# Optimization experiments

Hardware: AMD Instinct MI355X
Metric: run time of the kernel (lower is better)

The kernel has to match this reference:

```python
import jax, jax.numpy as jnp
import numpy as np

VOCAB, EMB, HID, NCLS = 50257, 48, 128, 2000
B, S = 512, 1024


def setup_inputs() -> dict:
    key = jax.random.key(0)
    ks = jax.random.split(key, 8)
    x = jax.random.randint(ks[0], (B, S), 0, VOCAB)
    emb_table = jax.random.normal(ks[1], (VOCAB, EMB), dtype=jnp.float32)
    emb_table = emb_table.at[0].set(0.0)  # padding_idx=0
    k_ih = 1.0 / np.sqrt(HID)
    w_ih = jax.random.uniform(ks[2], (4 * HID, EMB), minval=-k_ih, maxval=k_ih, dtype=jnp.float32)
    w_hh = jax.random.uniform(ks[3], (4 * HID, HID), minval=-k_ih, maxval=k_ih, dtype=jnp.float32)
    b_ih = jax.random.uniform(ks[4], (4 * HID,), minval=-k_ih, maxval=k_ih, dtype=jnp.float32)
    b_hh = jax.random.uniform(ks[5], (4 * HID,), minval=-k_ih, maxval=k_ih, dtype=jnp.float32)
    k_fc = 1.0 / np.sqrt(HID)
    w_fc = jax.random.uniform(ks[6], (NCLS, HID), minval=-k_fc, maxval=k_fc, dtype=jnp.float32)
    b_fc = jax.random.uniform(ks[7], (NCLS,), minval=-k_fc, maxval=k_fc, dtype=jnp.float32)
    return {"x": x, "emb_table": emb_table, "w_ih": w_ih, "w_hh": w_hh,
            "b_ih": b_ih, "b_hh": b_hh, "w_fc": w_fc, "b_fc": b_fc}


def _lstm_last_hidden(e, w_ih, w_hh, b_ih, b_hh):
    # e: [B, S, E]. Precompute input contributions for all timesteps (one big GEMM).
    xg = jnp.einsum('bse,ge->bsg', e, w_ih) + b_ih + b_hh  # [B, S, 4H]
    xg = jnp.transpose(xg, (1, 0, 2))                      # [S, B, 4H]
    Bn = e.shape[0]
    h0 = jnp.zeros((Bn, HID), e.dtype)
    c0 = jnp.zeros((Bn, HID), e.dtype)

    def step(carry, xg_t):
        h, c = carry
        g = xg_t + h @ w_hh.T                              # [B, 4H]
        i, f, gg, o = jnp.split(g, 4, axis=-1)             # PyTorch gate order i,f,g,o
        i = jax.nn.sigmoid(i)
        f = jax.nn.sigmoid(f)
        gg = jnp.tanh(gg)
        o = jax.nn.sigmoid(o)
        c = f * c + i * gg
        h = o * jnp.tanh(c)
        return (h, c), None

    (h_n, _), _ = jax.lax.scan(step, (h0, c0), xg)
    return h_n


def reference(x, emb_table, w_ih, w_hh, b_ih, b_hh, w_fc, b_fc):
    e = emb_table[x]                                       # [B, S, E] gather
    h_n = _lstm_last_hidden(e, w_ih, w_hh, b_ih, b_hh)     # [B, H]
    return h_n @ w_fc.T + b_fc                             # [B, NCLS]
```

## Files before the change

kernel.cpp:

```cpp
#include <hip/hip_runtime.h>

#define DI __device__ __forceinline__

typedef unsigned int uint;
typedef unsigned short ushort;
typedef _Float16 half2t __attribute__((ext_vector_type(2)));

#define VOCAB 50257
#define NEMB 48
#define HID 128
#define G4 512
#define NCLS 2000
#define BATCH 512
#define SEQ 1024

#if __has_builtin(__builtin_amdgcn_fdot2)
DI float fdot2(half2t a, half2t b, float c) { return __builtin_amdgcn_fdot2(a, b, c, false); }
#else
DI float fdot2(half2t a, half2t b, float c) { return c + (float)a.x * (float)b.x + (float)a.y * (float)b.y; }
#endif

#define LOG2E 1.4426950408889634f

DI float dppx1(float v) {
  return __builtin_bit_cast(float,
      __builtin_amdgcn_update_dpp(0, __builtin_bit_cast(int, v), 0xB1, 0xF, 0xF, true));
}
DI float dppx2(float v) {
  return __builtin_bit_cast(float,
      __builtin_amdgcn_update_dpp(0, __builtin_bit_cast(int, v), 0x4E, 0xF, 0xF, true));
}
DI float dppb3(float v) {
  return __builtin_bit_cast(float,
      __builtin_amdgcn_update_dpp(0, __builtin_bit_cast(int, v), 0xFF, 0xF, 0xF, true));
}

#define VROWS 32
__global__ __launch_bounds__(512) void build_P(
    const float* __restrict__ emb, const float* __restrict__ w_ih,
    const float* __restrict__ b_ih, const float* __restrict__ b_hh,
    ushort* __restrict__ P3)
{
  __shared__ __align__(16) float eL[VROWS][NEMB];
  const int tid = threadIdx.x;
  const int v0 = blockIdx.x * VROWS;
  int nrows = VOCAB - v0; if (nrows > VROWS) nrows = VROWS;

  for (int f = tid; f < nrows * NEMB; f += 512)
    eL[f / NEMB][f % NEMB] = emb[(size_t)v0 * NEMB + f];

  float w[NEMB];
  {
    const float* wr = w_ih + (size_t)tid * NEMB;
#pragma unroll
    for (int k = 0; k < NEMB; k++) w[k] = wr[k];
  }
  float bias = b_ih[tid] + b_hh[tid];
  __syncthreads();

  for (int v = 0; v < nrows; v++) {
    const float4* e4 = (const float4*)&eL[v][0];
    float a = bias;
#pragma unroll
    for (int k = 0; k < NEMB / 4; k++) {
      float4 e = e4[k];
      a += w[4 * k] * e.x + w[4 * k + 1] * e.y + w[4 * k + 2] * e.z + w[4 * k + 3] * e.w;
    }
    P3[(size_t)(v0 + v) * G4 + tid] = __builtin_bit_cast(ushort, (_Float16)a);
  }
}

template<bool USE_P>
__global__ __launch_bounds__(512, 4) void lstm_scan(
    const int* __restrict__ x, const float* __restrict__ emb,
    const float* __restrict__ w_ih, const float* __restrict__ w_hh,
    const float* __restrict__ b_ih, const float* __restrict__ b_hh,
    const ushort* __restrict__ P3, float* __restrict__ hout)
{
  __shared__ int tokL[SEQ];
  __shared__ __align__(16) _Float16 h16[2][HID];
  __shared__ __align__(8) half2t e16[2][NEMB / 2];

  const int tid = threadIdx.x;
  const int b   = blockIdx.x;
  const int u   = tid >> 2;
  const int q   = tid & 3;
  const bool par1 = (q & 1) != 0;
  const bool par2 = (q & 2) != 0;
  const int goff = (q << 7) + u;

  const bool isg = (q == 2);
  const float mk = isg ? (2.0f * LOG2E) : (-LOG2E);
  const float av = isg ? -2.0f : 1.0f;
  const float bv = isg ? 1.0f : 0.0f;

  {
    const int* xp = x + (size_t)b * SEQ;
    tokL[tid] = xp[tid];
    tokL[tid + 512] = xp[tid + 512];
  }

  half2t w[4][16];
#pragma unroll
  for (int g = 0; g < 4; g++) {
    const float4* wr = (const float4*)(w_hh + (size_t)(g * HID + u) * HID + 32 * q);
#pragma unroll
    for (int k4 = 0; k4 < 8; k4++) {
      float4 v = wr[k4];
      half2t p;
      p.x = (_Float16)v.x; p.y = (_Float16)v.y; w[g][2 * k4] = p;
      p.x = (_Float16)v.z; p.y = (_Float16)v.w; w[g][2 * k4 + 1] = p;
    }
  }

  half2t wihq[NEMB / 2];
  float biasq = 0.0f;
  if (!USE_P) {
    const float* wr = w_ih + (size_t)(q * HID + u) * NEMB;
#pragma unroll
    for (int k = 0; k < NEMB / 2; k++) {
      half2t p; p.x = (_Float16)wr[2 * k]; p.y = (_Float16)wr[2 * k + 1];
      wihq[k] = p;
    }
    biasq = b_ih[q * HID + u] + b_hh[q * HID + u];
  }
  if (tid < HID) h16[1][tid] = (_Float16)0.0f;
  __syncthreads();

  float c = 0.0f;
  ushort pa = 0, pb = 0;
  float2 einfl = {0.0f, 0.0f};
  if (USE_P) {
    pa = P3[(size_t)tokL[0] * G4 + goff];
    pb = P3[(size_t)tokL[1] * G4 + goff];
  } else {
    if (tid < NEMB / 2) {
      float2 e0 = ((const float2*)(emb + (size_t)tokL[0] * NEMB))[tid];
      einfl     = ((const float2*)(emb + (size_t)tokL[1] * NEMB))[tid];
      half2t p; p.x = (_Float16)e0.x; p.y = (_Float16)e0.y;
      e16[0][tid] = p;
    }
    __syncthreads();
  }

#define STEP(t, par) do {                                                      \
    int tc = (t) + 2; if (tc > SEQ - 1) tc = SEQ - 1;                          \
    int tn = tokL[tc];                                                         \
    ushort cur = (par) ? pb : pa;                                              \
    if (USE_P) {                                                               \
      ushort nx = P3[(size_t)tn * G4 + goff];                \
      if ((par) == 0) pa = nx; else pb = nx;                                   \
    } else {                                                                   \
      if (tid < NEMB / 2) {                                                    \
        half2t p; p.x = (_Float16)einfl.x; p.y = (_Float16)einfl.y;            \
        e16[((t) + 1) & 1][tid] = p;                                           \
        einfl = ((const float2*)(emb + (size_t)tn * NEMB))[tid];               \
      }                                                                        \
    }                                                                          \
    const uint4* hv = (const uint4*)(&h16[(par) ^ 1][32 * q]);                 \
    float a0 = 0.f, a1 = 0.f, a2 = 0.f, a3 = 0.f;                              \
    _Pragma("unroll")                                                          \
    for (int q4 = 0; q4 < 4; q4++) {                                           \
      uint4 hq = hv[q4];                                                       \
      half2t h0 = __builtin_bit_cast(half2t, hq.x);                            \
      half2t h1 = __builtin_bit_cast(half2t, hq.y);                            \
      half2t h2 = __builtin_bit_cast(half2t, hq.z);                            \
      half2t h3 = __builtin_bit_cast(half2t, hq.w);                            \
      a0 = fdot2(w[0][4*q4+0], h0, a0); a1 = fdot2(w[1][4*q4+0], h0, a1);      \
      a2 = fdot2(w[2][4*q4+0], h0, a2); a3 = fdot2(w[3][4*q4+0], h0, a3);      \
      a0 = fdot2(w[0][4*q4+1], h1, a0); a1 = fdot2(w[1][4*q4+1], h1, a1);      \
      a2 = fdot2(w[2][4*q4+1], h1, a2); a3 = fdot2(w[3][4*q4+1], h1, a3);      \
      a0 = fdot2(w[0][4*q4+2], h2, a0); a1 = fdot2(w[1][4*q4+2], h2, a1);      \
      a2 = fdot2(w[2][4*q4+2], h2, a2); a3 = fdot2(w[3][4*q4+2], h2, a3);      \
      a0 = fdot2(w[0][4*q4+3], h3, a0); a1 = fdot2(w[1][4*q4+3], h3, a1);      \
      a2 = fdot2(w[2][4*q4+3], h3, a2); a3 = fdot2(w[3][4*q4+3], h3, a3);      \
    }                                                                          \
                       \
    float kA = par1 ? a1 : a0, sA = par1 ? a0 : a1; kA += dppx1(sA);           \
    float kB = par1 ? a3 : a2, sB = par1 ? a2 : a3; kB += dppx1(sB);           \
    float kF = par2 ? kB : kA, sF = par2 ? kA : kB; kF += dppx2(sF);           \
    float xg;                                                                  \
    if (USE_P) {                                                               \
      xg = (float)__builtin_bit_cast(_Float16, cur);                           \
    } else {                                                                   \
      xg = biasq;                                                              \
      _Pragma("unroll")                                                        \
      for (int k = 0; k < NEMB / 2; k++) xg = fdot2(wihq[k], e16[(par)][k], xg);\
    }                                                                          \
    float gv = kF + xg;                                                        \
    float act = av * __builtin_amdgcn_rcpf(                                    \
                    __builtin_amdgcn_exp2f(mk * gv) + 1.0f) + bv;              \
    float gt = dppx2(act);                                 \
    float sf = dppx1(act);                                \
    c = act * gt + sf * c;                                \
    float tanhc = 1.0f - 2.0f * __builtin_amdgcn_rcpf(                         \
                    __builtin_amdgcn_exp2f(2.0f * LOG2E * c) + 1.0f);          \
    float so = dppb3(act);                            \
    float hh = so * tanhc;                                \
    if (q == 0) {                                                              \
      h16[(par)][u] = (_Float16)hh;                                            \
      if ((t) == SEQ - 1) hout[(size_t)b * HID + u] = hh;                      \
    }                                                                          \
    __syncthreads();                                                           \
  } while (0)

  for (int t = 0; t < SEQ; t += 2) { STEP(t, 0); STEP(t + 1, 1); }
#undef STEP
}

#define FCR 64
#define FCC 64
__global__ __launch_bounds__(256) void fc_kernel(
    const float* __restrict__ h, const float* __restrict__ w_fc,
    const float* __restrict__ b_fc, float* __restrict__ out)
{
  __shared__ float aT[HID][FCR];
  __shared__ float bT[HID][FCC];
  const int tid = threadIdx.x;
  const int r0 = blockIdx.y * FCR;
  const int c0 = blockIdx.x * FCC;

  for (int f = tid; f < FCR * (HID / 4); f += 256) {
    int row = f >> 5, qq = f & 31;
    float4 v = ((const float4*)h)[(((size_t)(r0 + row)) << 5) + qq];
    aT[4 * qq + 0][row] = v.x; aT[4 * qq + 1][row] = v.y;
    aT[4 * qq + 2][row] = v.z; aT[4 * qq + 3][row] = v.w;
    int wrow = c0 + row;
    float4 wv;
    if (wrow < NCLS) wv = ((const float4*)w_fc)[(((size_t)wrow) << 5) + qq];
    else { wv.x = 0.f; wv.y = 0.f; wv.z = 0.f; wv.w = 0.f; }
    bT[4 * qq + 0][row] = wv.x; bT[4 * qq + 1][row] = wv.y;
    bT[4 * qq + 2][row] = wv.z; bT[4 * qq + 3][row] = wv.w;
  }
  __syncthreads();

  const int cr = tid & 15, rr = tid >> 4;
  float acc[4][4];
#pragma unroll
  for (int i = 0; i < 4; i++)
#pragma unroll
    for (int j = 0; j < 4; j++) acc[i][j] = 0.0f;

#pragma unroll 4
  for (int k = 0; k < HID; k++) {
    float4 av = *(const float4*)&aT[k][4 * rr];
    float4 bv = *(const float4*)&bT[k][4 * cr];
    float a[4] = {av.x, av.y, av.z, av.w};
    float bb[4] = {bv.x, bv.y, bv.z, bv.w};
#pragma unroll
    for (int i = 0; i < 4; i++)
#pragma unroll
      for (int j = 0; j < 4; j++) acc[i][j] += a[i] * bb[j];
  }

#pragma unroll
  for (int j = 0; j < 4; j++) {
    int cc = c0 + 4 * cr + j;
    if (cc < NCLS) {
      float bias = b_fc[cc];
#pragma unroll
      for (int i = 0; i < 4; i++)
        out[(size_t)(r0 + 4 * rr + i) * NCLS + cc] = acc[i][j] + bias;
    }
  }
}

extern "C" void kernel_launch(void* const* d_in, const int* in_sizes, int n_in,
                              void* d_out, int out_size, void* d_ws, size_t ws_size,
                              hipStream_t stream) {
  const int*   xx   = (const int*)d_in[0];
  const float* emb  = (const float*)d_in[1];
  const float* w_ih = (const float*)d_in[2];
  const float* w_hh = (const float*)d_in[3];
  const float* b_ih = (const float*)d_in[4];
  const float* b_hh = (const float*)d_in[5];
  const float* w_fc = (const float*)d_in[6];
  const float* b_fc = (const float*)d_in[7];
  float* out = (float*)d_out;

  const size_t pbytes = (size_t)VOCAB * G4 * sizeof(ushort);
  const size_t palign = (pbytes + 255) & ~(size_t)255;
  const size_t hbytes = (size_t)BATCH * HID * sizeof(float);

  float* hout;
  if (ws_size >= palign + hbytes) {
    ushort* P3 = (ushort*)d_ws;
    hout = (float*)((char*)d_ws + palign);
    build_P<<<(VOCAB + VROWS - 1) / VROWS, 512, 0, stream>>>(emb, w_ih, b_ih, b_hh, P3);
    lstm_scan<true><<<BATCH, 512, 0, stream>>>(xx, emb, w_ih, w_hh, b_ih, b_hh, P3, hout);
  } else {
    hout = (float*)d_ws;
    lstm_scan<false><<<BATCH, 512, 0, stream>>>(xx, emb, w_ih, w_hh, b_ih, b_hh,
                                                (const ushort*)nullptr, hout);
  }
  dim3 fcg((NCLS + FCC - 1) / FCC, BATCH / FCR);
  fc_kernel<<<fcg, 256, 0, stream>>>(hout, w_fc, b_fc, out);
}
```

Baseline: 1.017 ms.

## Deepen P3 gather prefetch to four steps and use LDS-only barrier

The LSTM scan now prefetches the precomputed input-gate values four timesteps ahead instead of two, rotating through four registers in a loop unrolled by four. The token array is padded so the prefetch index needs no clamp. The per-step __syncthreads is replaced by an inline-asm barrier that waits only on LDS counters (lgkmcnt), so the outstanding global gather is not drained at every step. This hides more gather latency on the serial recurrence, but relies on the asm barrier being correct for the shared-memory h exchange and uses more registers.

```diff
diff --git a/kernel.cpp b/kernel.cpp
--- a/kernel.cpp
+++ b/kernel.cpp
@@ -34,6 +34,8 @@
   return __builtin_bit_cast(float,
       __builtin_amdgcn_update_dpp(0, __builtin_bit_cast(int, v), 0xFF, 0xF, 0xF, true));
 }
+
+DI void bar_lds() { asm volatile("s_waitcnt lgkmcnt(0)\n\ts_barrier" ::: "memory"); }
 
 #define VROWS 32
 __global__ __launch_bounds__(512) void build_P(
@@ -77,7 +79,7 @@
     const float* __restrict__ b_ih, const float* __restrict__ b_hh,
     const ushort* __restrict__ P3, float* __restrict__ hout)
 {
-  __shared__ int tokL[SEQ];
+  __shared__ int tokPad[SEQ + 4];
   __shared__ __align__(16) _Float16 h16[2][HID];
   __shared__ __align__(8) half2t e16[2][NEMB / 2];
 
@@ -96,8 +98,9 @@
 
   {
     const int* xp = x + (size_t)b * SEQ;
-    tokL[tid] = xp[tid];
-    tokL[tid + 512] = xp[tid + 512];
+    tokPad[tid] = xp[tid];
+    tokPad[tid + 512] = xp[tid + 512];
+    if (tid < 4) tokPad[SEQ + tid] = xp[SEQ - 1];
   }
 
   half2t w[4][16];
@@ -128,36 +131,36 @@
   __syncthreads();
 
   float c = 0.0f;
-  ushort pa = 0, pb = 0;
+  ushort pr0 = 0, pr1 = 0, pr2 = 0, pr3 = 0;
   float2 einfl = {0.0f, 0.0f};
   if (USE_P) {
-    pa = P3[(size_t)tokL[0] * G4 + goff];
-    pb = P3[(size_t)tokL[1] * G4 + goff];
+    pr0 = P3[(size_t)tokPad[0] * G4 + goff];
+    pr1 = P3[(size_t)tokPad[1] * G4 + goff];
+    pr2 = P3[(size_t)tokPad[2] * G4 + goff];
+    pr3 = P3[(size_t)tokPad[3] * G4 + goff];
   } else {
     if (tid < NEMB / 2) {
-      float2 e0 = ((const float2*)(emb + (size_t)tokL[0] * NEMB))[tid];
-      einfl     = ((const float2*)(emb + (size_t)tokL[1] * NEMB))[tid];
+      float2 e0 = ((const float2*)(emb + (size_t)tokPad[0] * NEMB))[tid];
+      einfl     = ((const float2*)(emb + (size_t)tokPad[1] * NEMB))[tid];
       half2t p; p.x = (_Float16)e0.x; p.y = (_Float16)e0.y;
       e16[0][tid] = p;
     }
     __syncthreads();
   }
 
-#define STEP(t, par) do {                                                      \
-    int tc = (t) + 2; if (tc > SEQ - 1) tc = SEQ - 1;                          \
-    int tn = tokL[tc];                                                         \
-    ushort cur = (par) ? pb : pa;                                              \
+#define STEP(tt, jpar, PRJ) do {                                               \
+    ushort cur = PRJ;                                                          \
     if (USE_P) {                                                               \
-      ushort nx = P3[(size_t)tn * G4 + goff];                \
-      if ((par) == 0) pa = nx; else pb = nx;                                   \
+      int tn4 = tokPad[(tt) + 4];                                              \
+      PRJ = P3[(size_t)tn4 * G4 + goff];           \
     } else {                                                                   \
       if (tid < NEMB / 2) {                                                    \
         half2t p; p.x = (_Float16)einfl.x; p.y = (_Float16)einfl.y;            \
-        e16[((t) + 1) & 1][tid] = p;                                           \
-        einfl = ((const float2*)(emb + (size_t)tn * NEMB))[tid];               \
+        e16[((tt) + 1) & 1][tid] = p;                                          \
+        einfl = ((const float2*)(emb + (size_t)tokPad[(tt) + 2] * NEMB))[tid]; \
       }                                                                        \
     }                                                                          \
-    const uint4* hv = (const uint4*)(&h16[(par) ^ 1][32 * q]);                 \
+    const uint4* hv = (const uint4*)(&h16[((jpar) + 1) & 1][32 * q]);          \
     float a0 = 0.f, a1 = 0.f, a2 = 0.f, a3 = 0.f;                              \
     _Pragma("unroll")                                                          \
     for (int q4 = 0; q4 < 4; q4++) {                                           \
@@ -185,7 +188,8 @@
     } else {                                                                   \
       xg = biasq;                                                              \
       _Pragma("unroll")                                                        \
-      for (int k = 0; k < NEMB / 2; k++) xg = fdot2(wihq[k], e16[(par)][k], xg);\
+      for (int k = 0; k < NEMB / 2; k++)                                       \
+        xg = fdot2(wihq[k], e16[(jpar) & 1][k], xg);                           \
     }                                                                          \
     float gv = kF + xg;                                                        \
     float act = av * __builtin_amdgcn_rcpf(                                    \
@@ -198,13 +202,18 @@
     float so = dppb3(act);                            \
     float hh = so * tanhc;                                \
     if (q == 0) {                                                              \
-      h16[(par)][u] = (_Float16)hh;                                            \
-      if ((t) == SEQ - 1) hout[(size_t)b * HID + u] = hh;                      \
+      h16[(jpar) & 1][u] = (_Float16)hh;                                       \
+      if ((tt) == SEQ - 1) hout[(size_t)b * HID + u] = hh;                     \
     }                                                                          \
-    __syncthreads();                                                           \
+    bar_lds();                                                                 \
   } while (0)
 
-  for (int t = 0; t < SEQ; t += 2) { STEP(t, 0); STEP(t + 1, 1); }
+  for (int t = 0; t < SEQ; t += 4) {
+    STEP(t, 0, pr0);
+    STEP(t + 1, 1, pr1);
+    STEP(t + 2, 2, pr2);
+    STEP(t + 3, 3, pr3);
+  }
 #undef STEP
 }
 
```

Result: no change. 1.004 ms (-1.3%).
